# Performance work log

Hardware: AMD Instinct MI355X
Metric: run time of the kernel (lower is better)

Reference implementation:

```python
import jax, jax.numpy as jnp
import numpy as np

LAPLACE_SCALE = 0.5


def setup_inputs() -> dict:
    key = jax.random.key(0)
    k1, k2, k3 = jax.random.split(key, 3)
    B, M, D = 8, 512, 64
    return {
        "k": jax.random.normal(k1, (B, M, D), dtype=jnp.float32),
        "v": jax.random.normal(k2, (B, M, D), dtype=jnp.float32),
        "q": jax.random.normal(k3, (B, M, D), dtype=jnp.float32),
    }


def reference(k, v, q):
    # Laplace attention branch (faithful to original, including comparing k to v):
    # k_: [B,1,M,D], v_: [B,M,1,D] -> unnorm: [B,M,M]
    unnorm = jnp.abs((k[:, None, :, :] - v[:, :, None, :]) * LAPLACE_SCALE).sum(axis=-1)
    weights = jax.nn.softmax(unnorm, axis=-1)  # [B,M,M]
    rep = jnp.einsum('bik,bkj->bij', weights, v)  # [B,M,D]
    return rep
```

## Files before the change

kernel.cpp:

```cpp
#include <hip/hip_runtime.h>


typedef _Float16 h2 __attribute__((ext_vector_type(2)));

#if __has_builtin(__builtin_amdgcn_fdot2)
#define FDOT2(a, b, c) __builtin_amdgcn_fdot2((a), (b), (c), false)
#else
static __device__ inline float FDOT2(h2 a, h2 b, float c) {
    return c + (float)a.x * (float)b.x + (float)a.y * (float)b.y;
}
#endif

#if __has_builtin(__builtin_amdgcn_sad_u16)
#define SADU16(a, b, c) __builtin_amdgcn_sad_u16((a), (b), (c))
#else
static __device__ inline unsigned SADU16(unsigned a, unsigned b, unsigned c) {
    const unsigned al = a & 0xFFFFu, ah = a >> 16;
    const unsigned bl = b & 0xFFFFu, bh = b >> 16;
    const unsigned dl = al > bl ? al - bl : bl - al;
    const unsigned dh = ah > bh ? ah - bh : bh - ah;
    return c + dl + dh;
}
#endif

static __device__ inline unsigned pk16(float x, float y) {
    h2 h;
    h.x = (_Float16)x;
    h.y = (_Float16)y;
    return __builtin_bit_cast(unsigned, h);
}

static __device__ inline unsigned q16(float x) {
    return (unsigned)(x * 4096.0f + 32768.5f);
}

constexpr int B_ = 8, M_ = 512, D_ = 64;
constexpr int GRID1 = 8 * 16 * 8;
#define C2L  1.761099911e-4f
#define CFIX 67.0f

constexpr int OFF_KH  = 0;
constexpr int OFF_VH  = 2176;
constexpr int OFF_VJ2 = 3328;
constexpr int OFF_WH  = 5504;
constexpr int OFF_DEN = 6528;
constexpr int LDS_U   = 6656;

static __device__ inline int cswz(int lane, int off) {
    return (off + 4 * ((lane >> 1) & 3)) & 15;
}

__global__ __launch_bounds__(256, 4)
void laplace_k1(const float* __restrict__ K, const float* __restrict__ V,
                unsigned* __restrict__ repH, float* __restrict__ den_part) {
    __shared__ __align__(16) unsigned lds[LDS_U];

    const int blk = blockIdx.x;
    const int b  = blk >> 7;
    const int it = (blk >> 3) & 15;
    const int jg = blk & 7;
    const int i0 = it * 32, j0 = jg * 64;

    const float* __restrict__ Kb = K + (size_t)b * (M_ * D_);
    const float* __restrict__ Vb = V + (size_t)b * (M_ * D_);

    const int t = threadIdx.x;

    const int rowK = t >> 2, dqK = t & 3;
    const int rowV = t >> 3, dqV = t & 7;
    const int j2s  = t >> 3;
    const int dcs  = (t & 7) * 8;

    const float* kp = Kb + (size_t)(j0 + rowK) * D_ + dqK * 16;
    const float* vp = Vb + (size_t)(i0 + rowV) * D_ + dqV * 8;
    const float* r0 = Vb + (size_t)(j0 + 2 * j2s) * D_ + dcs;
    const float* r1 = r0 + D_;

    float4 kq0 = *reinterpret_cast<const float4*>(kp);
    float4 kq1 = *reinterpret_cast<const float4*>(kp + 4);
    float4 kq2 = *reinterpret_cast<const float4*>(kp + 8);
    float4 kq3 = *reinterpret_cast<const float4*>(kp + 12);
    float4 vqa = *reinterpret_cast<const float4*>(vp);
    float4 vqb = *reinterpret_cast<const float4*>(vp + 4);
    float4 a0  = *reinterpret_cast<const float4*>(r0);
    float4 a1  = *reinterpret_cast<const float4*>(r0 + 4);
    float4 b0  = *reinterpret_cast<const float4*>(r1);
    float4 b1  = *reinterpret_cast<const float4*>(r1 + 4);

    {
        const float4 kqA[4] = {kq0, kq1, kq2, kq3};
#pragma unroll
        for (int c = 0; c < 4; ++c) {
            lds[OFF_KH + (dqK * 8 + 2 * c + 0) * 68 + rowK] =
                q16(kqA[c].x) | (q16(kqA[c].y) << 16);
            lds[OFF_KH + (dqK * 8 + 2 * c + 1) * 68 + rowK] =
                q16(kqA[c].z) | (q16(kqA[c].w) << 16);
        }
    }
    {
        lds[OFF_VH + (dqV * 4 + 0) * 36 + rowV] = q16(vqa.x) | (q16(vqa.y) << 16);
        lds[OFF_VH + (dqV * 4 + 1) * 36 + rowV] = q16(vqa.z) | (q16(vqa.w) << 16);
        lds[OFF_VH + (dqV * 4 + 2) * 36 + rowV] = q16(vqb.x) | (q16(vqb.y) << 16);
        lds[OFF_VH + (dqV * 4 + 3) * 36 + rowV] = q16(vqb.z) | (q16(vqb.w) << 16);
    }
    {
        *reinterpret_cast<uint4*>(&lds[OFF_VJ2 + j2s * 68 + dcs]) =
            make_uint4(pk16(a0.x, b0.x), pk16(a0.y, b0.y),
                       pk16(a0.z, b0.z), pk16(a0.w, b0.w));
        *reinterpret_cast<uint4*>(&lds[OFF_VJ2 + j2s * 68 + dcs + 4]) =
            make_uint4(pk16(a1.x, b1.x), pk16(a1.y, b1.y),
                       pk16(a1.z, b1.z), pk16(a1.w, b1.w));
    }
    __syncthreads();

    const int wv = t >> 6, lane = t & 63;
    const int ig = lane >> 2;
    const int jq = lane & 3;

    unsigned sacc[2][4];
#pragma unroll
    for (int a = 0; a < 2; ++a)
#pragma unroll
        for (int c = 0; c < 4; ++c) sacc[a][c] = 0u;

    const unsigned* pV = lds + OFF_VH + ig * 2;
    const unsigned* pK = lds + OFF_KH + wv * 16 + jq * 4;

#pragma unroll 8
    for (int d2 = 0; d2 < 32; ++d2) {
        const uint2 va = *reinterpret_cast<const uint2*>(pV + d2 * 36);
        const uint4 ka = *reinterpret_cast<const uint4*>(pK + d2 * 68);
        sacc[0][0] = SADU16(ka.x, va.x, sacc[0][0]);
        sacc[0][1] = SADU16(ka.y, va.x, sacc[0][1]);
        sacc[0][2] = SADU16(ka.z, va.x, sacc[0][2]);
        sacc[0][3] = SADU16(ka.w, va.x, sacc[0][3]);
        sacc[1][0] = SADU16(ka.x, va.y, sacc[1][0]);
        sacc[1][1] = SADU16(ka.y, va.y, sacc[1][1]);
        sacc[1][2] = SADU16(ka.z, va.y, sacc[1][2]);
        sacc[1][3] = SADU16(ka.w, va.y, sacc[1][3]);
    }

    float w[2][4], den[2];
#pragma unroll
    for (int a = 0; a < 2; ++a) {
        den[a] = 0.f;
#pragma unroll
        for (int c = 0; c < 4; ++c) {
            float e = exp2f((float)sacc[a][c] * C2L - CFIX);
            e = fminf(e, 60000.0f);
            w[a][c] = e;
            den[a] += e;
        }
        den[a] += __shfl_xor(den[a], 1);
        den[a] += __shfl_xor(den[a], 2);
    }
    float* dnl = reinterpret_cast<float*>(lds + OFF_DEN);
    if (jq == 0)
        *reinterpret_cast<float2*>(&dnl[wv * 32 + ig * 2]) = make_float2(den[0], den[1]);

    {
        unsigned* wH = lds + OFF_WH + wv * 256;
        const int j2 = jq * 2;
#pragma unroll
        for (int a = 0; a < 2; ++a) {
            wH[(j2 + 0) * 32 + ig * 2 + a] = pk16(w[a][0], w[a][1]);
            wH[(j2 + 1) * 32 + ig * 2 + a] = pk16(w[a][2], w[a][3]);
        }
    }

    const int ig3 = lane >> 3;
    const int dg  = lane & 7;

    float acc[4][8];
#pragma unroll
    for (int a = 0; a < 4; ++a)
#pragma unroll
        for (int c = 0; c < 8; ++c) acc[a][c] = 0.f;

    const unsigned* pW  = lds + OFF_WH + wv * 256 + ig3 * 4;
    const unsigned* pVJ = lds + OFF_VJ2 + (wv * 8) * 68 + dg * 8;

#pragma unroll
    for (int j2 = 0; j2 < 8; ++j2) {
        const uint4 wq = *reinterpret_cast<const uint4*>(pW + j2 * 32);
        const uint4 v0 = *reinterpret_cast<const uint4*>(pVJ + j2 * 68);
        const uint4 v1 = *reinterpret_cast<const uint4*>(pVJ + j2 * 68 + 4);
        const unsigned wA[4] = {wq.x, wq.y, wq.z, wq.w};
        const unsigned vA[8] = {v0.x, v0.y, v0.z, v0.w, v1.x, v1.y, v1.z, v1.w};
#pragma unroll
        for (int a = 0; a < 4; ++a) {
            const h2 wa = __builtin_bit_cast(h2, wA[a]);
#pragma unroll
            for (int c = 0; c < 8; ++c)
                acc[a][c] = FDOT2(wa, __builtin_bit_cast(h2, vA[c]), acc[a][c]);
        }
    }
    __syncthreads();

    {
        unsigned* cmb = lds + wv * 1024 + lane * 16;
#pragma unroll
        for (int a = 0; a < 4; ++a)
            *reinterpret_cast<uint4*>(cmb + cswz(lane, a * 4)) =
                make_uint4(pk16(acc[a][0], acc[a][1]), pk16(acc[a][2], acc[a][3]),
                           pk16(acc[a][4], acc[a][5]), pk16(acc[a][6], acc[a][7]));
    }
    __syncthreads();

    {
        const int i_  = t >> 3;
        const int dgr = t & 7;
        const int L   = ((i_ >> 2) << 3) + dgr;
        const int off = (i_ & 3) * 4;
        const int po  = cswz(L, off);

        float x[4] = {0.f, 0.f, 0.f, 0.f}, y[4] = {0.f, 0.f, 0.f, 0.f};
#pragma unroll
        for (int wq = 0; wq < 4; ++wq) {
            const uint4 q = *reinterpret_cast<const uint4*>(lds + wq * 1024 + L * 16 + po);
            const unsigned qa[4] = {q.x, q.y, q.z, q.w};
#pragma unroll
            for (int c = 0; c < 4; ++c) {
                const h2 h = __builtin_bit_cast(h2, qa[c]);
                x[c] += (float)h.x;
                y[c] += (float)h.y;
            }
        }
        *reinterpret_cast<uint4*>(repH + (size_t)blk * 1024 + t * 4) =
            make_uint4(pk16(x[0], y[0]), pk16(x[1], y[1]),
                       pk16(x[2], y[2]), pk16(x[3], y[3]));

        if (t < 32)
            den_part[(size_t)blk * 32 + t] =
                (dnl[t] + dnl[32 + t]) + (dnl[64 + t] + dnl[96 + t]);
    }
}

__global__ __launch_bounds__(256)
void laplace_k2(const unsigned* __restrict__ repH,
                const float* __restrict__ den_part,
                float2* __restrict__ out2) {
    const int gid = blockIdx.x * 256 + threadIdx.x;
    const int b   = gid >> 14;
    const int i9  = (gid >> 5) & 511;
    const int d2  = gid & 31;
    const int it  = i9 >> 5, il = i9 & 31;

    const size_t base = (size_t)(b * 16 + it) * 8;

    float dsum = 0.f;
#pragma unroll
    for (int s = 0; s < 8; ++s) dsum += den_part[(base + s) * 32 + il];

    float ax = 0.f, ay = 0.f;
    const unsigned* rp = repH + base * 1024 + (size_t)il * 32 + d2;
#pragma unroll
    for (int s = 0; s < 8; ++s) {
        const h2 h = __builtin_bit_cast(h2, rp[(size_t)s * 1024]);
        ax += (float)h.x;
        ay += (float)h.y;
    }
    const float inv = 1.0f / dsum;
    out2[gid] = make_float2(ax * inv, ay * inv);
}

extern "C" void kernel_launch(void* const* d_in, const int* in_sizes, int n_in,
                              void* d_out, int out_size, void* d_ws, size_t ws_size,
                              hipStream_t stream) {
    const float* K = (const float*)d_in[0];
    const float* V = (const float*)d_in[1];

    unsigned* repH = (unsigned*)d_ws;
    float*    den  = (float*)((char*)d_ws + 4 * 1024 * 1024);

    laplace_k1<<<dim3(GRID1), dim3(256), 0, stream>>>(K, V, repH, den);
    laplace_k2<<<dim3(512), dim3(256), 0, stream>>>(repH, den, (float2*)d_out);
}
```

Baseline: 17.10 us.

## Double j-tile per block to 128 with 512 threads, halving split-K partials

Each block of the first kernel now handles 128 key columns instead of 64, using 512 threads (8 waves), so the grid shrinks from 1024 to 512 blocks. The shared-memory layout, load mapping and cross-wave reduction are reworked for 8 waves. The second kernel only has to combine 4 partial results per row instead of 8. This cuts partial-result traffic and the reduction work, at the cost of fewer blocks, larger LDS use per block and a heavier in-block reduction.

```diff
diff --git a/kernel.cpp b/kernel.cpp
--- a/kernel.cpp
+++ b/kernel.cpp
@@ -35,31 +35,31 @@
 }
 
 constexpr int B_ = 8, M_ = 512, D_ = 64;
-constexpr int GRID1 = 8 * 16 * 8;
+constexpr int GRID1 = 8 * 16 * 4;
 #define C2L  1.761099911e-4f
 #define CFIX 67.0f
 
 constexpr int OFF_KH  = 0;
-constexpr int OFF_VH  = 2176;
-constexpr int OFF_VJ2 = 3328;
-constexpr int OFF_WH  = 5504;
-constexpr int OFF_DEN = 6528;
-constexpr int LDS_U   = 6656;
+constexpr int OFF_VH  = 4224;
+constexpr int OFF_VJ2 = 5376;
+constexpr int OFF_WH  = 9728;
+constexpr int OFF_DEN = 11776;
+constexpr int LDS_U   = 12032;
 
 static __device__ inline int cswz(int lane, int off) {
     return (off + 4 * ((lane >> 1) & 3)) & 15;
 }
 
-__global__ __launch_bounds__(256, 4)
+__global__ __launch_bounds__(512, 4)
 void laplace_k1(const float* __restrict__ K, const float* __restrict__ V,
                 unsigned* __restrict__ repH, float* __restrict__ den_part) {
     __shared__ __align__(16) unsigned lds[LDS_U];
 
     const int blk = blockIdx.x;
-    const int b  = blk >> 7;
-    const int it = (blk >> 3) & 15;
-    const int jg = blk & 7;
-    const int i0 = it * 32, j0 = jg * 64;
+    const int b  = blk >> 6;
+    const int it = (blk >> 2) & 15;
+    const int jg = blk & 3;
+    const int i0 = it * 32, j0 = jg * 128;
 
     const float* __restrict__ Kb = K + (size_t)b * (M_ * D_);
     const float* __restrict__ Vb = V + (size_t)b * (M_ * D_);
@@ -67,12 +67,12 @@
     const int t = threadIdx.x;
 
     const int rowK = t >> 2, dqK = t & 3;
-    const int rowV = t >> 3, dqV = t & 7;
+    const int rowV = t >> 4, dqV = t & 15;
     const int j2s  = t >> 3;
     const int dcs  = (t & 7) * 8;
 
     const float* kp = Kb + (size_t)(j0 + rowK) * D_ + dqK * 16;
-    const float* vp = Vb + (size_t)(i0 + rowV) * D_ + dqV * 8;
+    const float* vp = Vb + (size_t)(i0 + rowV) * D_ + dqV * 4;
     const float* r0 = Vb + (size_t)(j0 + 2 * j2s) * D_ + dcs;
     const float* r1 = r0 + D_;
 
@@ -80,8 +80,7 @@
     float4 kq1 = *reinterpret_cast<const float4*>(kp + 4);
     float4 kq2 = *reinterpret_cast<const float4*>(kp + 8);
     float4 kq3 = *reinterpret_cast<const float4*>(kp + 12);
-    float4 vqa = *reinterpret_cast<const float4*>(vp);
-    float4 vqb = *reinterpret_cast<const float4*>(vp + 4);
+    float4 vq  = *reinterpret_cast<const float4*>(vp);
     float4 a0  = *reinterpret_cast<const float4*>(r0);
     float4 a1  = *reinterpret_cast<const float4*>(r0 + 4);
     float4 b0  = *reinterpret_cast<const float4*>(r1);
@@ -91,17 +90,15 @@
         const float4 kqA[4] = {kq0, kq1, kq2, kq3};
 #pragma unroll
         for (int c = 0; c < 4; ++c) {
-            lds[OFF_KH + (dqK * 8 + 2 * c + 0) * 68 + rowK] =
+            lds[OFF_KH + (dqK * 8 + 2 * c + 0) * 132 + rowK] =
                 q16(kqA[c].x) | (q16(kqA[c].y) << 16);
-            lds[OFF_KH + (dqK * 8 + 2 * c + 1) * 68 + rowK] =
+            lds[OFF_KH + (dqK * 8 + 2 * c + 1) * 132 + rowK] =
                 q16(kqA[c].z) | (q16(kqA[c].w) << 16);
         }
     }
     {
-        lds[OFF_VH + (dqV * 4 + 0) * 36 + rowV] = q16(vqa.x) | (q16(vqa.y) << 16);
-        lds[OFF_VH + (dqV * 4 + 1) * 36 + rowV] = q16(vqa.z) | (q16(vqa.w) << 16);
-        lds[OFF_VH + (dqV * 4 + 2) * 36 + rowV] = q16(vqb.x) | (q16(vqb.y) << 16);
-        lds[OFF_VH + (dqV * 4 + 3) * 36 + rowV] = q16(vqb.z) | (q16(vqb.w) << 16);
+        lds[OFF_VH + (dqV * 2 + 0) * 36 + rowV] = q16(vq.x) | (q16(vq.y) << 16);
+        lds[OFF_VH + (dqV * 2 + 1) * 36 + rowV] = q16(vq.z) | (q16(vq.w) << 16);
     }
     {
         *reinterpret_cast<uint4*>(&lds[OFF_VJ2 + j2s * 68 + dcs]) =
@@ -129,7 +126,7 @@
 #pragma unroll 8
     for (int d2 = 0; d2 < 32; ++d2) {
         const uint2 va = *reinterpret_cast<const uint2*>(pV + d2 * 36);
-        const uint4 ka = *reinterpret_cast<const uint4*>(pK + d2 * 68);
+        const uint4 ka = *reinterpret_cast<const uint4*>(pK + d2 * 132);
         sacc[0][0] = SADU16(ka.x, va.x, sacc[0][0]);
         sacc[0][1] = SADU16(ka.y, va.x, sacc[0][1]);
         sacc[0][2] = SADU16(ka.z, va.x, sacc[0][2]);
@@ -208,31 +205,32 @@
     __syncthreads();
 
     {
-        const int i_  = t >> 3;
-        const int dgr = t & 7;
+        const int i_  = t >> 4;
+        const int q   = t & 15;
+        const int dgr = q >> 1;
+        const int cc  = (q & 1) * 2;
         const int L   = ((i_ >> 2) << 3) + dgr;
         const int off = (i_ & 3) * 4;
-        const int po  = cswz(L, off);
-
-        float x[4] = {0.f, 0.f, 0.f, 0.f}, y[4] = {0.f, 0.f, 0.f, 0.f};
-#pragma unroll
-        for (int wq = 0; wq < 4; ++wq) {
-            const uint4 q = *reinterpret_cast<const uint4*>(lds + wq * 1024 + L * 16 + po);
-            const unsigned qa[4] = {q.x, q.y, q.z, q.w};
-#pragma unroll
-            for (int c = 0; c < 4; ++c) {
-                const h2 h = __builtin_bit_cast(h2, qa[c]);
-                x[c] += (float)h.x;
-                y[c] += (float)h.y;
-            }
-        }
-        *reinterpret_cast<uint4*>(repH + (size_t)blk * 1024 + t * 4) =
-            make_uint4(pk16(x[0], y[0]), pk16(x[1], y[1]),
-                       pk16(x[2], y[2]), pk16(x[3], y[3]));
-
-        if (t < 32)
-            den_part[(size_t)blk * 32 + t] =
-                (dnl[t] + dnl[32 + t]) + (dnl[64 + t] + dnl[96 + t]);
+        const int po  = cswz(L, off) + cc;
+
+        float x0 = 0.f, y0 = 0.f, x1 = 0.f, y1 = 0.f;
+#pragma unroll
+        for (int wq = 0; wq < 8; ++wq) {
+            const uint2 u = *reinterpret_cast<const uint2*>(lds + wq * 1024 + L * 16 + po);
+            const h2 ha = __builtin_bit_cast(h2, u.x);
+            const h2 hb = __builtin_bit_cast(h2, u.y);
+            x0 += (float)ha.x; y0 += (float)ha.y;
+            x1 += (float)hb.x; y1 += (float)hb.y;
+        }
+        *reinterpret_cast<uint2*>(repH + (size_t)blk * 1024 + i_ * 32 + q * 2) =
+            make_uint2(pk16(x0, y0), pk16(x1, y1));
+
+        if (t < 32) {
+            float ds = 0.f;
+#pragma unroll
+            for (int wq = 0; wq < 8; ++wq) ds += dnl[wq * 32 + t];
+            den_part[(size_t)blk * 32 + t] = ds;
+        }
     }
 }
 
@@ -246,16 +244,16 @@
     const int d2  = gid & 31;
     const int it  = i9 >> 5, il = i9 & 31;
 
-    const size_t base = (size_t)(b * 16 + it) * 8;
+    const size_t base = (size_t)(b * 16 + it) * 4;
 
     float dsum = 0.f;
 #pragma unroll
-    for (int s = 0; s < 8; ++s) dsum += den_part[(base + s) * 32 + il];
+    for (int s = 0; s < 4; ++s) dsum += den_part[(base + s) * 32 + il];
 
     float ax = 0.f, ay = 0.f;
     const unsigned* rp = repH + base * 1024 + (size_t)il * 32 + d2;
 #pragma unroll
-    for (int s = 0; s < 8; ++s) {
+    for (int s = 0; s < 4; ++s) {
         const h2 h = __builtin_bit_cast(h2, rp[(size_t)s * 1024]);
         ax += (float)h.x;
         ay += (float)h.y;
@@ -271,8 +269,8 @@
     const float* V = (const float*)d_in[1];
 
     unsigned* repH = (unsigned*)d_ws;
-    float*    den  = (float*)((char*)d_ws + 4 * 1024 * 1024);
-
-    laplace_k1<<<dim3(GRID1), dim3(256), 0, stream>>>(K, V, repH, den);
+    float*    den  = (float*)((char*)d_ws + 2 * 1024 * 1024);
+
+    laplace_k1<<<dim3(GRID1), dim3(512), 0, stream>>>(K, V, repH, den);
     laplace_k2<<<dim3(512), dim3(256), 0, stream>>>(repH, den, (float2*)d_out);
 }
```

Measured after the change: 16.17 us (median of 2 runs). -5.4%, faster.
